# Kernel tuning notes

Measured on AMD Instinct MI355X. Metric: run time of the kernel, lower is better.

## Reference

```python
import jax, jax.numpy as jnp
import numpy as np

V, BLK, C, H, L = 50257, 1024, 1024, 16, 4
B, T = 2, 1024
D = C // H
EPS = 1e-5

def _ln(x, w):
    mu = jnp.mean(x, axis=-1, keepdims=True)
    var = jnp.mean(jnp.square(x - mu), axis=-1, keepdims=True)
    return (x - mu) * jax.lax.rsqrt(var + EPS) * w

def setup_inputs() -> dict:
    key = jax.random.key(0)
    ks = jax.random.split(key, 9)
    s = 0.02
    return {
        'idx': jax.random.randint(ks[0], (B, T), 0, V),
        'wte': jax.random.normal(ks[1], (V, C), jnp.float32) * s,
        'wpe': jax.random.normal(ks[2], (BLK, C), jnp.float32) * s,
        'ln1_w': jnp.ones((L, C), jnp.float32),
        'attn_w': jax.random.normal(ks[3], (L, 3 * C, C), jnp.float32) * s,   # torch Linear [out,in]
        'attnproj_w': jax.random.normal(ks[4], (L, C, C), jnp.float32) * (s / np.sqrt(2 * L)),
        'ln2_w': jnp.ones((L, C), jnp.float32),
        'fc_w': jax.random.normal(ks[5], (L, 4 * C, C), jnp.float32) * s,
        'mlpproj_w': jax.random.normal(ks[6], (L, C, 4 * C), jnp.float32) * (s / np.sqrt(2 * L)),
        'lnf_w': jnp.ones((C,), jnp.float32),
        'head_w': jax.random.normal(ks[7], (V, C), jnp.float32) * s,
    }

def _block(x, ln1_w, attn_w, attnproj_w, ln2_w, fc_w, mlpproj_w):
    b, t, c = x.shape
    h = _ln(x, ln1_w)
    qkv = h @ attn_w.T                                  # [B,T,3C]
    q, k, v = jnp.split(qkv, 3, axis=-1)
    q = q.reshape(b, t, H, D).transpose(0, 2, 1, 3)      # [B,H,T,D]
    k = k.reshape(b, t, H, D).transpose(0, 2, 1, 3)
    v = v.reshape(b, t, H, D).transpose(0, 2, 1, 3)
    att = jnp.einsum('bhqd,bhkd->bhqk', q, k) * (1.0 / np.sqrt(D))
    causal = jnp.tril(jnp.ones((t, t), bool))
    att = jnp.where(causal, att, jnp.float32(-jnp.inf))
    p = jax.nn.softmax(att, axis=-1)
    y = jnp.einsum('bhqk,bhkd->bhqd', p, v)
    y = y.transpose(0, 2, 1, 3).reshape(b, t, c)
    y = y @ attnproj_w.T
    x = x + y
    m = _ln(x, ln2_w)
    m = jax.nn.relu(m @ fc_w.T) @ mlpproj_w.T
    return x + m

def reference(idx, wte, wpe, ln1_w, attn_w, attnproj_w, ln2_w, fc_w, mlpproj_w, lnf_w, head_w):
    t = idx.shape[1]
    x = wte[idx] + wpe[:t]                               # [B,T,C]
    for i in range(L):
        x = _block(x, ln1_w[i], attn_w[i], attnproj_w[i], ln2_w[i], fc_w[i], mlpproj_w[i])
    x = _ln(x, lnf_w)
    return x @ head_w.T                                  # logits [B,T,V]
```

## Files before the change

### kernel.cpp

```cpp
#include <hip/hip_runtime.h>

typedef __bf16 bf16x8 __attribute__((ext_vector_type(8)));
typedef float f32x4 __attribute__((ext_vector_type(4)));
typedef unsigned short u16x8 __attribute__((ext_vector_type(8)));

#define LOG2E 1.4426950408889634f

__device__ __forceinline__ unsigned short f2bf(float f) {
  union { float f; unsigned u; } v; v.f = f;
  return (unsigned short)((v.u + 0x7fffu + ((v.u >> 16) & 1u)) >> 16);
}

__device__ __forceinline__ void gload16(const void* g, void* l) {
  __builtin_amdgcn_global_load_lds(
      (const __attribute__((address_space(1))) unsigned int*)g,
      (__attribute__((address_space(3))) unsigned int*)l, 16, 0, 0);
}

__global__ __launch_bounds__(256) void cvt_kernel(
    const float* __restrict__ s, unsigned short* __restrict__ d, int n8) {
  int i = blockIdx.x * 256 + threadIdx.x;
  int stride = gridDim.x * 256;
  for (; i < n8; i += stride) {
    float4 a = ((const float4*)s)[2 * i];
    float4 b = ((const float4*)s)[2 * i + 1];
    u16x8 o;
    o[0] = f2bf(a.x); o[1] = f2bf(a.y); o[2] = f2bf(a.z); o[3] = f2bf(a.w);
    o[4] = f2bf(b.x); o[5] = f2bf(b.y); o[6] = f2bf(b.z); o[7] = f2bf(b.w);
    ((u16x8*)d)[i] = o;
  }
}

__global__ __launch_bounds__(256) void embed_kernel(
    const int* __restrict__ idx, const float* __restrict__ wte,
    const float* __restrict__ wpe, float* __restrict__ x) {
  int row = blockIdx.x;
  int tok = idx[row];
  int t = row & 1023;
  float4 a = ((const float4*)(wte + (size_t)tok * 1024))[threadIdx.x];
  float4 p = ((const float4*)(wpe + (size_t)t * 1024))[threadIdx.x];
  a.x += p.x; a.y += p.y; a.z += p.z; a.w += p.w;
  ((float4*)(x + (size_t)row * 1024))[threadIdx.x] = a;
}

__global__ __launch_bounds__(256) void ln_kernel(
    const float* __restrict__ x, const float* __restrict__ w,
    unsigned short* __restrict__ out) {
  __shared__ float2 red[4];
  int row = blockIdx.x, tid = threadIdx.x;
  float4 v = ((const float4*)(x + (size_t)row * 1024))[tid];
  float s  = v.x + v.y + v.z + v.w;
  float s2 = v.x * v.x + v.y * v.y + v.z * v.z + v.w * v.w;
#pragma unroll
  for (int m = 32; m >= 1; m >>= 1) {
    s  += __shfl_xor(s, m, 64);
    s2 += __shfl_xor(s2, m, 64);
  }
  if ((tid & 63) == 0) red[tid >> 6] = make_float2(s, s2);
  __syncthreads();
  float S = 0.f, S2 = 0.f;
#pragma unroll
  for (int i = 0; i < 4; ++i) { S += red[i].x; S2 += red[i].y; }
  float mu = S * (1.f / 1024.f);
  float var = S2 * (1.f / 1024.f) - mu * mu;
  float rs = rsqrtf(var + 1e-5f);
  float4 wv = ((const float4*)w)[tid];
  ushort4 o;
  o.x = f2bf((v.x - mu) * rs * wv.x);
  o.y = f2bf((v.y - mu) * rs * wv.y);
  o.z = f2bf((v.z - mu) * rs * wv.z);
  o.w = f2bf((v.w - mu) * rs * wv.w);
  ((ushort4*)(out + (size_t)row * 1024))[tid] = o;
}

template <int MODE, bool WB16>
__global__ __launch_bounds__(256, 2) void gemm_bt(
    const unsigned short* __restrict__ A, const void* __restrict__ Wp,
    void* __restrict__ outp, const float* __restrict__ resid,
    unsigned short* __restrict__ qo, unsigned short* __restrict__ ko,
    unsigned short* __restrict__ vo, int M, int N, int K) {
  __shared__ unsigned short As[2][128 * 64];
  __shared__ unsigned short Bs[2][128 * 64];

  const int tid = threadIdx.x;
  const int lane = tid & 63;
  const int wv = tid >> 6;
  const int lr = lane & 15, lh = lane >> 4;
  const int nbm = M >> 7;
  const int nb = gridDim.x;
  const int bid = blockIdx.x;
  const int swz = (bid & 7) * (nb >> 3) + (bid >> 3);
  const int m0 = (swz % nbm) << 7;
  const int n0 = (swz / nbm) << 7;
  const int wm = (wv >> 1) << 6;
  const int wn = (wv & 1) << 6;
  const int nK = K >> 6;

  float4 breg[8];
  const float* Wf = (const float*)Wp;
  const unsigned short* Wb = (const unsigned short*)Wp;

  auto loadB = [&](int kt) {
#pragma unroll
    for (int j = 0; j < 8; ++j) {
      int u = j * 256 + tid;
      int rn = n0 + (u >> 4);
      if (rn >= N) rn = N - 1;
      breg[j] = *(const float4*)(Wf + (size_t)rn * K + kt * 64 + (u & 15) * 4);
    }
  };
  auto writeB = [&](int buf) {
#pragma unroll
    for (int j = 0; j < 8; ++j) {
      int u = j * 256 + tid;
      int row = u >> 4, q = u & 15;
      ushort4 h4;
      h4.x = f2bf(breg[j].x); h4.y = f2bf(breg[j].y);
      h4.z = f2bf(breg[j].z); h4.w = f2bf(breg[j].w);
      int off = row * 128 + ((q * 8) ^ ((row & 7) << 4));
      *(ushort4*)((char*)(&Bs[buf][0]) + off) = h4;
    }
  };
  auto stageA = [&](int buf, int kt) {
    const unsigned short* base = A + (size_t)m0 * K + kt * 64;
#pragma unroll
    for (int j = 0; j < 4; ++j) {
      int u = j * 256 + tid;
      int row = u >> 3, un = u & 7;
      gload16(base + (size_t)row * K + ((un ^ (row & 7)) << 3),
              (char*)(&As[buf][0]) + u * 16);
    }
  };
  auto stageB16 = [&](int buf, int kt) {
#pragma unroll
    for (int j = 0; j < 4; ++j) {
      int u = j * 256 + tid;
      int row = u >> 3, un = u & 7;
      size_t grow = (size_t)(n0 + row);
      if constexpr (MODE == 4) { if ((int)grow >= N) grow = N - 1; }
      gload16(Wb + grow * K + kt * 64 + ((un ^ (row & 7)) << 3),
              (char*)(&Bs[buf][0]) + u * 16);
    }
  };

  f32x4 acc[4][4];
#pragma unroll
  for (int a = 0; a < 4; ++a)
#pragma unroll
    for (int b = 0; b < 4; ++b) acc[a][b] = f32x4{0.f, 0.f, 0.f, 0.f};

  if constexpr (WB16) {
    stageA(0, 0);
    stageB16(0, 0);
  } else {
    loadB(0);
    stageA(0, 0);
    writeB(0);
  }
  __syncthreads();

  for (int kt = 0; kt < nK; ++kt) {
    int cur = kt & 1;
    if constexpr (WB16) {
      if (kt + 1 < nK) { stageA(cur ^ 1, kt + 1); stageB16(cur ^ 1, kt + 1); }
    } else {
      if (kt + 1 < nK) { loadB(kt + 1); stageA(cur ^ 1, kt + 1); }
    }

    bf16x8 af[4][2], bf[4][2];
#pragma unroll
    for (int mi = 0; mi < 4; ++mi)
#pragma unroll
      for (int ks = 0; ks < 2; ++ks) {
        int row = wm + mi * 16 + lr;
        int off = row * 128 + ((ks * 64 + lh * 16) ^ ((row & 7) << 4));
        af[mi][ks] = *(const bf16x8*)((const char*)(&As[cur][0]) + off);
      }
#pragma unroll
    for (int ni = 0; ni < 4; ++ni)
#pragma unroll
      for (int ks = 0; ks < 2; ++ks) {
        int row = wn + ni * 16 + lr;
        int off = row * 128 + ((ks * 64 + lh * 16) ^ ((row & 7) << 4));
        bf[ni][ks] = *(const bf16x8*)((const char*)(&Bs[cur][0]) + off);
      }
#pragma unroll
    for (int ks = 0; ks < 2; ++ks)
#pragma unroll
      for (int mi = 0; mi < 4; ++mi)
#pragma unroll
        for (int ni = 0; ni < 4; ++ni)
          acc[mi][ni] = __builtin_amdgcn_mfma_f32_16x16x32_bf16(
              af[mi][ks], bf[ni][ks], acc[mi][ni], 0, 0, 0);

    if constexpr (!WB16) {
      if (kt + 1 < nK) writeB(cur ^ 1);
    }
    __syncthreads();
  }

#pragma unroll
  for (int mi = 0; mi < 4; ++mi)
#pragma unroll
    for (int ni = 0; ni < 4; ++ni)
#pragma unroll
      for (int r = 0; r < 4; ++r) {
        int grow = m0 + wm + mi * 16 + lh * 4 + r;
        int gcol = n0 + wn + ni * 16 + lr;
        float val = acc[mi][ni][r];
        if constexpr (MODE == 1) val = fmaxf(val, 0.f);
        if constexpr (MODE == 0 || MODE == 1) {
          ((unsigned short*)outp)[(size_t)grow * N + gcol] = f2bf(val);
        } else if constexpr (MODE == 2) {
          ((float*)outp)[(size_t)grow * N + gcol] =
              resid[(size_t)grow * N + gcol] + val;
        } else if constexpr (MODE == 3) {
          int which = gcol >> 10, hh = (gcol >> 6) & 15, dd = gcol & 63;
          int b = grow >> 10, t = grow & 1023;
          unsigned short hv = f2bf(val);
          size_t bh = (size_t)(b * 16 + hh) << 16;
          if (which == 0)      qo[bh + t * 64 + dd] = hv;
          else if (which == 1) ko[bh + t * 64 + dd] = hv;
          else                 vo[bh + dd * 1024 + t] = hv;
        } else {
          if (gcol < N)
            ((float*)outp)[(size_t)grow * (size_t)N + gcol] = val;
        }
      }
}

__global__ __launch_bounds__(256, 2) void attn_kernel(
    const unsigned short* __restrict__ qb, const unsigned short* __restrict__ kb,
    const unsigned short* __restrict__ vt, unsigned short* __restrict__ yb) {
  __shared__ unsigned short Ks[2][64 * 64];
  __shared__ unsigned short Vs[2][64 * 64];
  __shared__ unsigned short Ps[4][32 * 64];

  const int tid = threadIdx.x, lane = tid & 63, wv = tid >> 6;
  const int lr = lane & 15, lh = lane >> 4;
  const int bid = blockIdx.x;
  const int bh = bid >> 3, qt = bid & 7;
  const int q0 = qt << 7;
  const unsigned short* qp = qb + ((size_t)bh << 16);
  const unsigned short* kp = kb + ((size_t)bh << 16);
  const unsigned short* vp = vt + ((size_t)bh << 16);

  bf16x8 qf[2][2];
#pragma unroll
  for (int mi = 0; mi < 2; ++mi)
#pragma unroll
    for (int ks = 0; ks < 2; ++ks) {
      int row = q0 + wv * 32 + mi * 16 + lr;
      qf[mi][ks] = *(const bf16x8*)(qp + (size_t)row * 64 + ks * 32 + lh * 8);
    }

  f32x4 o[2][4];
  float mr[2][4], lsum[2][4];
#pragma unroll
  for (int mi = 0; mi < 2; ++mi) {
#pragma unroll
    for (int di = 0; di < 4; ++di) o[mi][di] = f32x4{0.f, 0.f, 0.f, 0.f};
#pragma unroll
    for (int r = 0; r < 4; ++r) { mr[mi][r] = -1e30f; lsum[mi][r] = 0.f; }
  }

  const int wqmax = q0 + wv * 32 + 31;
  const int ntiles = (q0 + 128) >> 6;

  auto stageKV = [&](int buf, int t) {
    int kv0 = t << 6;
#pragma unroll
    for (int j = 0; j < 2; ++j) {
      int u = j * 256 + tid;
      int row = u >> 3, un = u & 7;
      gload16(kp + (size_t)(kv0 + row) * 64 + ((un ^ (row & 7)) << 3),
              (char*)(&Ks[buf][0]) + u * 16);
      gload16(vp + (size_t)row * 1024 + kv0 + ((un ^ (row & 7)) << 3),
              (char*)(&Vs[buf][0]) + u * 16);
    }
  };

  stageKV(0, 0);

  for (int t = 0; t < ntiles; ++t) {
    __syncthreads();
    if (t + 1 < ntiles) stageKV((t + 1) & 1, t + 1);
    int cur = t & 1;
    int kv0 = t << 6;
    if (kv0 <= wqmax) {
      f32x4 s[2][4];
#pragma unroll
      for (int mi = 0; mi < 2; ++mi)
#pragma unroll
        for (int ni = 0; ni < 4; ++ni) s[mi][ni] = f32x4{0.f, 0.f, 0.f, 0.f};

      bf16x8 kf[4][2];
#pragma unroll
      for (int ni = 0; ni < 4; ++ni)
#pragma unroll
        for (int ks = 0; ks < 2; ++ks) {
          int row = ni * 16 + lr;
          int off = row * 128 + ((ks * 64 + lh * 16) ^ ((row & 7) << 4));
          kf[ni][ks] = *(const bf16x8*)((const char*)(&Ks[cur][0]) + off);
        }
#pragma unroll
      for (int ks = 0; ks < 2; ++ks)
#pragma unroll
        for (int mi = 0; mi < 2; ++mi)
#pragma unroll
          for (int ni = 0; ni < 4; ++ni)
            s[mi][ni] = __builtin_amdgcn_mfma_f32_16x16x32_bf16(
                qf[mi][ks], kf[ni][ks], s[mi][ni], 0, 0, 0);

#pragma unroll
      for (int mi = 0; mi < 2; ++mi)
#pragma unroll
        for (int r = 0; r < 4; ++r) {
          int rowq = q0 + wv * 32 + mi * 16 + lh * 4 + r;
          float xv[4];
          float pm = -1e30f;
#pragma unroll
          for (int ni = 0; ni < 4; ++ni) {
            int col = kv0 + ni * 16 + lr;
            float xx = s[mi][ni][r] * 0.125f;
            if (col > rowq) xx = -1e30f;
            xv[ni] = xx;
            pm = fmaxf(pm, xx);
          }
#pragma unroll
          for (int msk = 1; msk < 16; msk <<= 1)
            pm = fmaxf(pm, __shfl_xor(pm, msk, 64));
          float mnew = fmaxf(mr[mi][r], pm);
          float al = exp2f((mr[mi][r] - mnew) * LOG2E);
          mr[mi][r] = mnew;
          float ps = 0.f;
#pragma unroll
          for (int ni = 0; ni < 4; ++ni) {
            float p = exp2f((xv[ni] - mnew) * LOG2E);
            s[mi][ni][r] = p;
            ps += p;
          }
#pragma unroll
          for (int msk = 1; msk < 16; msk <<= 1) ps += __shfl_xor(ps, msk, 64);
          lsum[mi][r] = lsum[mi][r] * al + ps;
#pragma unroll
          for (int di = 0; di < 4; ++di) o[mi][di][r] *= al;
        }

#pragma unroll
      for (int mi = 0; mi < 2; ++mi)
#pragma unroll
        for (int ni = 0; ni < 4; ++ni)
#pragma unroll
          for (int r = 0; r < 4; ++r) {
            int row = mi * 16 + lh * 4 + r;
            int off = row * 128 + (((ni * 16 + lr) * 2) ^ ((row & 7) << 4));
            *(unsigned short*)((char*)(&Ps[wv][0]) + off) = f2bf(s[mi][ni][r]);
          }

      bf16x8 pf[2][2], vf[4][2];
#pragma unroll
      for (int mi = 0; mi < 2; ++mi)
#pragma unroll
        for (int ks = 0; ks < 2; ++ks) {
          int row = mi * 16 + lr;
          int off = row * 128 + ((ks * 64 + lh * 16) ^ ((row & 7) << 4));
          pf[mi][ks] = *(const bf16x8*)((const char*)(&Ps[wv][0]) + off);
        }
#pragma unroll
      for (int di = 0; di < 4; ++di)
#pragma unroll
        for (int ks = 0; ks < 2; ++ks) {
          int row = di * 16 + lr;
          int off = row * 128 + ((ks * 64 + lh * 16) ^ ((row & 7) << 4));
          vf[di][ks] = *(const bf16x8*)((const char*)(&Vs[cur][0]) + off);
        }
#pragma unroll
      for (int ks = 0; ks < 2; ++ks)
#pragma unroll
        for (int mi = 0; mi < 2; ++mi)
#pragma unroll
          for (int di = 0; di < 4; ++di)
            o[mi][di] = __builtin_amdgcn_mfma_f32_16x16x32_bf16(
                pf[mi][ks], vf[di][ks], o[mi][di], 0, 0, 0);
    }
  }

  int b = bh >> 4, hh = bh & 15;
#pragma unroll
  for (int mi = 0; mi < 2; ++mi)
#pragma unroll
    for (int r = 0; r < 4; ++r) {
      float inv = 1.f / lsum[mi][r];
      int rowq = q0 + wv * 32 + mi * 16 + lh * 4 + r;
      size_t mg = (size_t)(b * 1024 + rowq) * 1024 + hh * 64;
#pragma unroll
      for (int di = 0; di < 4; ++di)
        yb[mg + di * 16 + lr] = f2bf(o[mi][di][r] * inv);
    }
}

extern "C" void kernel_launch(void* const* d_in, const int* in_sizes, int n_in,
                              void* d_out, int out_size, void* d_ws,
                              size_t ws_size, hipStream_t stream) {
  const int*   idx  = (const int*)d_in[0];
  const float* wte  = (const float*)d_in[1];
  const float* wpe  = (const float*)d_in[2];
  const float* ln1w = (const float*)d_in[3];
  const float* attnw= (const float*)d_in[4];
  const float* aprj = (const float*)d_in[5];
  const float* ln2w = (const float*)d_in[6];
  const float* fcw  = (const float*)d_in[7];
  const float* mprj = (const float*)d_in[8];
  const float* lnfw = (const float*)d_in[9];
  const float* hw   = (const float*)d_in[10];
  float* out = (float*)d_out;
  char* ws = (char*)d_ws;

  float* x            = (float*)ws;
  unsigned short* h   = (unsigned short*)(ws + ((size_t)8 << 20));
  unsigned short* qbf = (unsigned short*)(ws + ((size_t)12 << 20));
  unsigned short* kbf = (unsigned short*)(ws + ((size_t)16 << 20));
  unsigned short* vtb = (unsigned short*)(ws + ((size_t)20 << 20));
  unsigned short* ybf = (unsigned short*)(ws + ((size_t)24 << 20));
  unsigned short* mhb = (unsigned short*)(ws + ((size_t)12 << 20));

  size_t off = (size_t)28 << 20;
  unsigned short* attnw16 = (unsigned short*)(ws + off); off += (size_t)4 * 3072 * 1024 * 2;
  unsigned short* aprj16  = (unsigned short*)(ws + off); off += (size_t)4 * 1024 * 1024 * 2;
  unsigned short* fcw16   = (unsigned short*)(ws + off); off += (size_t)4 * 4096 * 1024 * 2;
  unsigned short* mprj16  = (unsigned short*)(ws + off); off += (size_t)4 * 1024 * 4096 * 2;
  unsigned short* hw16    = (unsigned short*)(ws + off); off += (size_t)50257 * 1024 * 2;
  const bool b16 = ws_size >= off;

  embed_kernel<<<2048, 256, 0, stream>>>(idx, wte, wpe, x);

  if (b16) {
    cvt_kernel<<<2048, 256, 0, stream>>>(attnw, attnw16, 4 * 3072 * 1024 / 8);
    cvt_kernel<<<2048, 256, 0, stream>>>(aprj,  aprj16,  4 * 1024 * 1024 / 8);
    cvt_kernel<<<2048, 256, 0, stream>>>(fcw,   fcw16,   4 * 4096 * 1024 / 8);
    cvt_kernel<<<2048, 256, 0, stream>>>(mprj,  mprj16,  4 * 1024 * 4096 / 8);
    cvt_kernel<<<2048, 256, 0, stream>>>(hw,    hw16,    50257 * 1024 / 8);
  }

  for (int l = 0; l < 4; ++l) {
    ln_kernel<<<2048, 256, 0, stream>>>(x, ln1w + l * 1024, h);
    if (b16)
      gemm_bt<3, true><<<16 * 24, 256, 0, stream>>>(
          h, attnw16 + (size_t)l * 3072 * 1024, nullptr, nullptr, qbf, kbf,
          vtb, 2048, 3072, 1024);
    else
      gemm_bt<3, false><<<16 * 24, 256, 0, stream>>>(
          h, attnw + (size_t)l * 3072 * 1024, nullptr, nullptr, qbf, kbf, vtb,
          2048, 3072, 1024);
    attn_kernel<<<256, 256, 0, stream>>>(qbf, kbf, vtb, ybf);
    if (b16)
      gemm_bt<2, true><<<16 * 8, 256, 0, stream>>>(
          ybf, aprj16 + (size_t)l * 1024 * 1024, x, x, nullptr, nullptr,
          nullptr, 2048, 1024, 1024);
    else
      gemm_bt<2, false><<<16 * 8, 256, 0, stream>>>(
          ybf, aprj + (size_t)l * 1024 * 1024, x, x, nullptr, nullptr, nullptr,
          2048, 1024, 1024);
    ln_kernel<<<2048, 256, 0, stream>>>(x, ln2w + l * 1024, h);
    if (b16)
      gemm_bt<1, true><<<16 * 32, 256, 0, stream>>>(
          h, fcw16 + (size_t)l * 4096 * 1024, mhb, nullptr, nullptr, nullptr,
          nullptr, 2048, 4096, 1024);
    else
      gemm_bt<1, false><<<16 * 32, 256, 0, stream>>>(
          h, fcw + (size_t)l * 4096 * 1024, mhb, nullptr, nullptr, nullptr,
          nullptr, 2048, 4096, 1024);
    if (b16)
      gemm_bt<2, true><<<16 * 8, 256, 0, stream>>>(
          mhb, mprj16 + (size_t)l * 1024 * 4096, x, x, nullptr, nullptr,
          nullptr, 2048, 1024, 4096);
    else
      gemm_bt<2, false><<<16 * 8, 256, 0, stream>>>(
          mhb, mprj + (size_t)l * 1024 * 4096, x, x, nullptr, nullptr, nullptr,
          2048, 1024, 4096);
  }

  ln_kernel<<<2048, 256, 0, stream>>>(x, lnfw, h);
  if (b16)
    gemm_bt<4, true><<<16 * 393, 256, 0, stream>>>(
        h, hw16, out, nullptr, nullptr, nullptr, nullptr, 2048, 50257, 1024);
  else
    gemm_bt<4, false><<<16 * 393, 256, 0, stream>>>(
        h, hw, out, nullptr, nullptr, nullptr, nullptr, 2048, 50257, 1024);
}
```

Measured before the change: 1.452 ms.

## Add 256x256-tile 4-stage pipelined GEMM for the LM head projection

Adds a dedicated bf16 GEMM kernel with 256x256 output tiles, 512 threads, XOR-swizzled LDS, a 4-buffer async global-to-LDS pipeline and grid swizzling, and uses it for the vocabulary head GEMM when bf16 weights are available. Larger tiles raise arithmetic intensity and cut redundant loads of the 2048x1024 activation and the 50257x1024 head weights, which dominate this GEMM. The cost is very high register pressure (128 accumulator floats per thread) and a 128 KB shared-memory footprint, both of which limit occupancy. There is also tile waste on the ragged N edge, which clamps rows and masks stores.

```diff
diff --git a/kernel.cpp b/kernel.cpp
--- a/kernel.cpp
+++ b/kernel.cpp
@@ -226,6 +226,113 @@
           if (gcol < N)
             ((float*)outp)[(size_t)grow * (size_t)N + gcol] = val;
         }
+      }
+}
+
+__global__ __launch_bounds__(512, 2) void gemm256_bt(
+    const unsigned short* __restrict__ A, const unsigned short* __restrict__ Wb,
+    float* __restrict__ out, int M, int N, int K) {
+  __shared__ unsigned short As[4][256 * 32];
+  __shared__ unsigned short Bs[4][256 * 32];
+
+  const int tid = threadIdx.x;
+  const int lane = tid & 63;
+  const int wv = tid >> 6;
+  const int lr = lane & 15, lh = lane >> 4;
+  const int wm = (wv >> 2) * 128;
+  const int wn = (wv & 3) * 64;
+  const int nbm = M >> 8;
+  const int nb = gridDim.x;
+  const int bid = blockIdx.x;
+  const int swz = (bid & 7) * (nb >> 3) + (bid >> 3);
+  const int m0 = (swz % nbm) << 8;
+  const int n0 = (swz / nbm) << 8;
+  const int nK = K >> 5;
+
+  size_t aoff[2], boff[2];
+  int ldst[2];
+#pragma unroll
+  for (int j = 0; j < 2; ++j) {
+    int u = j * 512 + tid;
+    int p = u >> 3, s = u & 7;
+    int ss = s ^ (p & 7);
+    int arow = m0 + 2 * p + (ss >> 2);
+    int brow = n0 + 2 * p + (ss >> 2);
+    if (brow >= N) brow = N - 1;
+    aoff[j] = (size_t)arow * K + (ss & 3) * 8;
+    boff[j] = (size_t)brow * K + (ss & 3) * 8;
+    ldst[j] = u * 16;
+  }
+
+  auto stage = [&](int buf, int k) {
+#pragma unroll
+    for (int j = 0; j < 2; ++j)
+      gload16(A + aoff[j] + k * 32, (char*)(&As[buf][0]) + ldst[j]);
+#pragma unroll
+    for (int j = 0; j < 2; ++j)
+      gload16(Wb + boff[j] + k * 32, (char*)(&Bs[buf][0]) + ldst[j]);
+  };
+
+  f32x4 acc[8][4];
+#pragma unroll
+  for (int a = 0; a < 8; ++a)
+#pragma unroll
+    for (int b = 0; b < 4; ++b) acc[a][b] = f32x4{0.f, 0.f, 0.f, 0.f};
+
+  stage(0, 0);
+  if (nK > 1) stage(1, 1);
+  if (nK > 2) stage(2, 2);
+  if (nK > 2) asm volatile("s_waitcnt vmcnt(8)" ::: "memory");
+  else        asm volatile("s_waitcnt vmcnt(0)" ::: "memory");
+  __builtin_amdgcn_s_barrier();
+  __builtin_amdgcn_sched_barrier(0);
+
+  for (int k = 0; k < nK; ++k) {
+    const int buf = k & 3;
+    bf16x8 af[8], bfr[4];
+#pragma unroll
+    for (int ni = 0; ni < 4; ++ni) {
+      int r = wn + ni * 16 + lr;
+      int p = r >> 1;
+      int off = p * 128 + (((((r & 1) << 2) | lh) ^ (p & 7)) << 4);
+      bfr[ni] = *(const bf16x8*)((const char*)(&Bs[buf][0]) + off);
+    }
+#pragma unroll
+    for (int mi = 0; mi < 8; ++mi) {
+      int r = wm + mi * 16 + lr;
+      int p = r >> 1;
+      int off = p * 128 + (((((r & 1) << 2) | lh) ^ (p & 7)) << 4);
+      af[mi] = *(const bf16x8*)((const char*)(&As[buf][0]) + off);
+    }
+    if (k + 3 < nK) stage((k + 3) & 3, k + 3);
+
+    __builtin_amdgcn_s_setprio(1);
+#pragma unroll
+    for (int mi = 0; mi < 8; ++mi)
+#pragma unroll
+      for (int ni = 0; ni < 4; ++ni)
+        acc[mi][ni] = __builtin_amdgcn_mfma_f32_16x16x32_bf16(
+            af[mi], bfr[ni], acc[mi][ni], 0, 0, 0);
+    __builtin_amdgcn_s_setprio(0);
+
+    if (k + 1 < nK) {
+      if (k + 4 <= nK)      asm volatile("s_waitcnt vmcnt(8)" ::: "memory");
+      else if (k + 3 <= nK) asm volatile("s_waitcnt vmcnt(4)" ::: "memory");
+      else                  asm volatile("s_waitcnt vmcnt(0)" ::: "memory");
+      __builtin_amdgcn_s_barrier();
+      __builtin_amdgcn_sched_barrier(0);
+    }
+  }
+
+#pragma unroll
+  for (int mi = 0; mi < 8; ++mi)
+#pragma unroll
+    for (int ni = 0; ni < 4; ++ni)
+#pragma unroll
+      for (int r = 0; r < 4; ++r) {
+        int grow = m0 + wm + mi * 16 + lh * 4 + r;
+        int gcol = n0 + wn + ni * 16 + lr;
+        if (gcol < N) out[(size_t)grow * (size_t)N + gcol] = acc[mi][ni][r];
       }
 }
 
@@ -483,8 +590,7 @@
 
   ln_kernel<<<2048, 256, 0, stream>>>(x, lnfw, h);
   if (b16)
-    gemm_bt<4, true><<<16 * 393, 256, 0, stream>>>(
-        h, hw16, out, nullptr, nullptr, nullptr, nullptr, 2048, 50257, 1024);
+    gemm256_bt<<<8 * 197, 512, 0, stream>>>(h, hw16, out, 2048, 50257, 1024);
   else
     gemm_bt<4, false><<<16 * 393, 256, 0, stream>>>(
         h, hw, out, nullptr, nullptr, nullptr, nullptr, 2048, 50257, 1024);
```

Result: faster. 1.372 ms (-5.5%).
